# Kernel optimization log

Hardware: AMD Instinct MI355X
Metric: run time of the kernel (lower is better)

## Reference

```python
import jax, jax.numpy as jnp
import numpy as np


def setup_inputs() -> dict:
    key = jax.random.key(0)
    k1, k2, k3 = jax.random.split(key, 3)
    B, T = 4096, 8192
    X = jax.random.normal(k1, (B, T), dtype=jnp.float32)
    raw_a = jax.random.normal(k2, (), dtype=jnp.float32)
    raw_b = jax.random.normal(k3, (), dtype=jnp.float32)
    return {"X": X, "raw_a": raw_a, "raw_b": raw_b}


def reference(X, raw_a, raw_b):
    # project: a = 0.5*tanh(raw_a); per-step input u_t = a * x_t
    # forward step: z_t = u_t + b * z_{t-1},  b = tanh(raw_b),  z_0 = 0
    # readout: squeeze the size-1 hidden dim (already scalar here)
    a = 0.5 * jnp.tanh(raw_a)
    b = jnp.tanh(raw_b)
    u = a * X                      # [B, T]
    mult = jnp.full_like(u, b)     # constant decay per step

    # Affine composition: (m1, s1) then (m2, s2) -> (m2*m1, m2*s1 + s2)
    def combine(c1, c2):
        m1, s1 = c1
        m2, s2 = c2
        return (m1 * m2, m2 * s1 + s2)

    _, Z = jax.lax.associative_scan(combine, (mult, u), axis=1)
    return Z  # [B, T] hidden states over all timesteps
```

## Files before the change

### kernel.cpp

```cpp
#include <hip/hip_runtime.h>
#include <hip/hip_bf16.h>
#include <math.h>


#define T_LEN  8192
#define EPT    8
#define CHUNK  (64 * EPT)
#define NCHUNK (T_LEN / CHUNK)

__global__ __launch_bounds__(256) void lincell_scan(
    const float* __restrict__ X,
    const float* __restrict__ pa,
    const float* __restrict__ pb,
    float* __restrict__ Z,
    int nrows)
{
    const int gtid = blockIdx.x * blockDim.x + threadIdx.x;
    const int row  = gtid >> 6;
    const int lane = threadIdx.x & 63;
    if (row >= nrows) return;

    const float a = 0.5f * tanhf(pa[0]);
    const float b = tanhf(pb[0]);

    const float b2 = b  * b;
    const float b3 = b2 * b;
    const float b4 = b2 * b2;
    const float b5 = b4 * b;
    const float b6 = b4 * b2;
    const float b7 = b4 * b3;
    const float b8 = b4 * b4;

    float mstep[6];
#pragma unroll
    for (int k = 0; k < 6; ++k) {
        const int d = 1 << k;
        const int e = (lane + 1 < d) ? (lane + 1) : d;
        mstep[k] = powf(b8, (float)e);
    }
    const float b8lane = powf(b8, (float)lane);
    const float cdecay = powf(b8, 64.0f);

    const float* xrow = X + (size_t)row * T_LEN;
    float*       zrow = Z + (size_t)row * T_LEN;

    float carry = 0.0f;

#pragma unroll 2
    for (int c = 0; c < NCHUNK; ++c) {
        const float4* px = reinterpret_cast<const float4*>(xrow + (size_t)c * CHUNK) + (lane * 2);
        const float4 v0 = px[0];
        const float4 v1 = px[1];

        const float y0 = a * v0.x;
        const float y1 = fmaf(b, y0, a * v0.y);
        const float y2 = fmaf(b, y1, a * v0.z);
        const float y3 = fmaf(b, y2, a * v0.w);
        const float y4 = fmaf(b, y3, a * v1.x);
        const float y5 = fmaf(b, y4, a * v1.y);
        const float y6 = fmaf(b, y5, a * v1.z);
        const float y7 = fmaf(b, y6, a * v1.w);

        float s = y7;
#pragma unroll
        for (int k = 0; k < 6; ++k) {
            float t = __shfl_up(s, (unsigned)(1 << k), 64);
            t = (lane >= (1 << k)) ? t : 0.0f;
            s = fmaf(mstep[k], t, s);
        }

        float excl = __shfl_up(s, 1u, 64);
        excl = (lane >= 1) ? excl : 0.0f;
        const float pre = fmaf(b8lane, carry, excl);

        float4 o0, o1;
        o0.x = fmaf(b,  pre, y0);
        o0.y = fmaf(b2, pre, y1);
        o0.z = fmaf(b3, pre, y2);
        o0.w = fmaf(b4, pre, y3);
        o1.x = fmaf(b5, pre, y4);
        o1.y = fmaf(b6, pre, y5);
        o1.z = fmaf(b7, pre, y6);
        o1.w = fmaf(b8, pre, y7);

        float4* pz = reinterpret_cast<float4*>(zrow + (size_t)c * CHUNK) + (lane * 2);
        pz[0] = o0;
        pz[1] = o1;

        const float last = __shfl(s, 63, 64);
        carry = fmaf(cdecay, carry, last);
    }
}

extern "C" void kernel_launch(void* const* d_in, const int* in_sizes, int n_in,
                              void* d_out, int out_size, void* d_ws, size_t ws_size,
                              hipStream_t stream) {
    const float* X  = (const float*)d_in[0];
    const float* pa = (const float*)d_in[1];
    const float* pb = (const float*)d_in[2];
    float* Z = (float*)d_out;

    const int nrows = in_sizes[0] / T_LEN;
    const int waves_per_block = 4;
    const int blocks = (nrows + waves_per_block - 1) / waves_per_block;
    lincell_scan<<<blocks, 256, 0, stream>>>(X, pa, pb, Z, nrows);
}
```

Before: 238.8 us.

## Interleave four independent wave scans per chunk with register prefetch and nontemporal stores

Each wave now handles 1024-element chunks as four 256-element sub-chunks. A lane holds 4 contiguous elements per sub-chunk and the four shuffle scans run interleaved to expose ILP. The next chunk's loads are prefetched into registers while the current one is computed, and outputs use nontemporal stores to avoid cache pollution. The chunk loop is fully unrolled and more data is held in registers, so register pressure rises and occupancy may drop.

```diff
diff --git a/kernel.cpp b/kernel.cpp
--- a/kernel.cpp
+++ b/kernel.cpp
@@ -1,11 +1,12 @@
 #include <hip/hip_runtime.h>
-#include <hip/hip_bf16.h>
 #include <math.h>
 
 
+typedef float f32x4 __attribute__((ext_vector_type(4)));
+
 #define T_LEN  8192
-#define EPT    8
-#define CHUNK  (64 * EPT)
+#define NSUB   4
+#define CHUNK  1024
 #define NCHUNK (T_LEN / CHUNK)
 
 __global__ __launch_bounds__(256) void lincell_scan(
@@ -20,75 +21,84 @@
     const int lane = threadIdx.x & 63;
     if (row >= nrows) return;
 
-    const float a = 0.5f * tanhf(pa[0]);
-    const float b = tanhf(pb[0]);
-
-    const float b2 = b  * b;
+    const float a  = 0.5f * tanhf(pa[0]);
+    const float b  = tanhf(pb[0]);
+    const float b2 = b * b;
     const float b3 = b2 * b;
     const float b4 = b2 * b2;
-    const float b5 = b4 * b;
-    const float b6 = b4 * b2;
-    const float b7 = b4 * b3;
-    const float b8 = b4 * b4;
 
     float mstep[6];
 #pragma unroll
     for (int k = 0; k < 6; ++k) {
         const int d = 1 << k;
         const int e = (lane + 1 < d) ? (lane + 1) : d;
-        mstep[k] = powf(b8, (float)e);
+        mstep[k] = powf(b4, (float)e);
     }
-    const float b8lane = powf(b8, (float)lane);
-    const float cdecay = powf(b8, 64.0f);
+    const float b4lane = powf(b4, (float)lane);
+    const float bsub   = powf(b4, 64.0f);
 
-    const float* xrow = X + (size_t)row * T_LEN;
-    float*       zrow = Z + (size_t)row * T_LEN;
+    const f32x4* xrow = (const f32x4*)(X + (size_t)row * T_LEN);
+    f32x4*       zrow = (f32x4*)(Z + (size_t)row * T_LEN);
 
     float carry = 0.0f;
 
-#pragma unroll 2
+    f32x4 cur[NSUB];
+#pragma unroll
+    for (int j = 0; j < NSUB; ++j) cur[j] = xrow[j * 64 + lane];
+
+#pragma unroll
     for (int c = 0; c < NCHUNK; ++c) {
-        const float4* px = reinterpret_cast<const float4*>(xrow + (size_t)c * CHUNK) + (lane * 2);
-        const float4 v0 = px[0];
-        const float4 v1 = px[1];
+        f32x4 nxt[NSUB];
+        if (c + 1 < NCHUNK) {
+#pragma unroll
+            for (int j = 0; j < NSUB; ++j)
+                nxt[j] = xrow[(c + 1) * 256 + j * 64 + lane];
+        }
 
-        const float y0 = a * v0.x;
-        const float y1 = fmaf(b, y0, a * v0.y);
-        const float y2 = fmaf(b, y1, a * v0.z);
-        const float y3 = fmaf(b, y2, a * v0.w);
-        const float y4 = fmaf(b, y3, a * v1.x);
-        const float y5 = fmaf(b, y4, a * v1.y);
-        const float y6 = fmaf(b, y5, a * v1.z);
-        const float y7 = fmaf(b, y6, a * v1.w);
+        float y0[NSUB], y1[NSUB], y2[NSUB], y3[NSUB], s[NSUB];
+#pragma unroll
+        for (int j = 0; j < NSUB; ++j) {
+            y0[j] = a * cur[j].x;
+            y1[j] = fmaf(b, y0[j], a * cur[j].y);
+            y2[j] = fmaf(b, y1[j], a * cur[j].z);
+            y3[j] = fmaf(b, y2[j], a * cur[j].w);
+            s[j]  = y3[j];
+        }
 
-        float s = y7;
 #pragma unroll
         for (int k = 0; k < 6; ++k) {
-            float t = __shfl_up(s, (unsigned)(1 << k), 64);
-            t = (lane >= (1 << k)) ? t : 0.0f;
-            s = fmaf(mstep[k], t, s);
+#pragma unroll
+            for (int j = 0; j < NSUB; ++j) {
+                float t = __shfl_up(s[j], (unsigned)(1 << k), 64);
+                t = (lane >= (1 << k)) ? t : 0.0f;
+                s[j] = fmaf(mstep[k], t, s[j]);
+            }
         }
 
-        float excl = __shfl_up(s, 1u, 64);
-        excl = (lane >= 1) ? excl : 0.0f;
-        const float pre = fmaf(b8lane, carry, excl);
+        float excl[NSUB], tot[NSUB];
+#pragma unroll
+        for (int j = 0; j < NSUB; ++j) {
+            float e = __shfl_up(s[j], 1u, 64);
+            excl[j] = (lane >= 1) ? e : 0.0f;
+            tot[j]  = __shfl(s[j], 63, 64);
+        }
 
-        float4 o0, o1;
-        o0.x = fmaf(b,  pre, y0);
-        o0.y = fmaf(b2, pre, y1);
-        o0.z = fmaf(b3, pre, y2);
-        o0.w = fmaf(b4, pre, y3);
-        o1.x = fmaf(b5, pre, y4);
-        o1.y = fmaf(b6, pre, y5);
-        o1.z = fmaf(b7, pre, y6);
-        o1.w = fmaf(b8, pre, y7);
+        float cj = carry;
+#pragma unroll
+        for (int j = 0; j < NSUB; ++j) {
+            const float pre = fmaf(b4lane, cj, excl[j]);
+            f32x4 o;
+            o.x = fmaf(b,  pre, y0[j]);
+            o.y = fmaf(b2, pre, y1[j]);
+            o.z = fmaf(b3, pre, y2[j]);
+            o.w = fmaf(b4, pre, y3[j]);
+            __builtin_nontemporal_store(o, &zrow[c * 256 + j * 64 + lane]);
+            cj = fmaf(bsub, cj, tot[j]);
+        }
+        carry = cj;
 
-        float4* pz = reinterpret_cast<float4*>(zrow + (size_t)c * CHUNK) + (lane * 2);
-        pz[0] = o0;
-        pz[1] = o1;
-
-        const float last = __shfl(s, 63, 64);
-        carry = fmaf(cdecay, carry, last);
+#pragma unroll
+        for (int j = 0; j < NSUB; ++j) cur[j] = nxt[j];
     }
 }
 
@@ -101,7 +111,6 @@
     float* Z = (float*)d_out;
 
     const int nrows = in_sizes[0] / T_LEN;
-    const int waves_per_block = 4;
-    const int blocks = (nrows + waves_per_block - 1) / waves_per_block;
+    const int blocks = (nrows + 3) / 4;
     lincell_scan<<<blocks, 256, 0, stream>>>(X, pa, pb, Z, nrows);
 }
```

Measured after the change: 236.0 us. About the same (-1.2%).
